# Performance work log

Hardware: AMD Instinct MI355X
Metric: run time of the kernel (lower is better)

The kernel has to match this reference:

```python
import jax, jax.numpy as jnp
import numpy as np

N_SOURCES = 100000
N_SENSORS = 306
N_TIMES = 256
N_FEATURES = 8
HIDDEN = 128
N_LAYERS = 3
N_EDGES = 600000
TIKHONOV_REG = 1e-3


def setup_inputs() -> dict:
    key = jax.random.key(0)
    ks = jax.random.split(key, 16)
    scale = 1.0 / np.sqrt(HIDDEN)
    in_dim = N_FEATURES + N_TIMES
    return {
        "Y": jax.random.normal(ks[0], (N_SENSORS, N_TIMES), dtype=jnp.float32),
        "L": jax.random.normal(ks[1], (N_SENSORS, N_SOURCES), dtype=jnp.float32),
        "vertex_features": jax.random.normal(ks[2], (N_SOURCES, N_FEATURES), dtype=jnp.float32),
        "senders": jax.random.randint(ks[3], (N_EDGES,), 0, N_SOURCES, dtype=jnp.int32),
        "receivers": jax.random.randint(ks[4], (N_EDGES,), 0, N_SOURCES, dtype=jnp.int32),
        # eqx.nn.Linear params: weight (out, in), bias (out,)
        "W_in": jax.random.normal(ks[5], (HIDDEN, in_dim), dtype=jnp.float32) / np.sqrt(in_dim),
        "b_in": jnp.zeros((HIDDEN,), dtype=jnp.float32),
        # GraphConvLayer params, stacked over layers; applied as x @ W (no transpose)
        "W_self": jax.random.normal(ks[6], (N_LAYERS, HIDDEN, HIDDEN), dtype=jnp.float32) * scale,
        "W_msg": jax.random.normal(ks[7], (N_LAYERS, HIDDEN, HIDDEN), dtype=jnp.float32) * scale,
        "b_layer": jnp.zeros((N_LAYERS, HIDDEN), dtype=jnp.float32),
        "W_out": jax.random.normal(ks[8], (N_TIMES, HIDDEN), dtype=jnp.float32) / np.sqrt(HIDDEN),
        "b_out": jnp.zeros((N_TIMES,), dtype=jnp.float32),
    }


def _tikhonov_inverse(Y, L, reg):
    # J = V @ diag(s / (s^2 + reg^2)) @ U^T @ Y
    U, s, Vt = jnp.linalg.svd(L, full_matrices=False)
    filt = s / (s ** 2 + reg ** 2)
    return Vt.T @ (filt[:, None] * (U.T @ Y))  # (n_sources, n_times)


def _graph_conv(x, senders, receivers, W_self, W_msg, b):
    n_nodes = x.shape[0]
    messages = x[senders]                                   # (E, H) gather
    agg = jnp.zeros_like(x).at[receivers].add(messages)     # (N, H) scatter-add
    degree = jnp.zeros((n_nodes,), x.dtype).at[receivers].add(1.0)
    msg_mean = agg / jnp.maximum(degree, 1.0)[:, None]
    return jax.nn.relu(x @ W_self + msg_mean @ W_msg + b)


def reference(Y, L, vertex_features, senders, receivers,
              W_in, b_in, W_self, W_msg, b_layer, W_out, b_out):
    J0 = _tikhonov_inverse(Y, L, TIKHONOV_REG)              # (N, T)
    x = jnp.concatenate([J0, vertex_features], axis=1)      # (N, T + F)
    x = x @ W_in.T + b_in                                   # vmap(Linear)
    for i in range(N_LAYERS):
        x = _graph_conv(x, senders, receivers, W_self[i], W_msg[i], b_layer[i])
    J = x @ W_out.T + b_out                                 # (N, T)
    return J
```

## Files before the change

### kernel.cpp

```cpp
#include <hip/hip_runtime.h>

#define NSRC 100000
#define NSEN 306
#define NT 256
#define NF 8
#define NH 128
#define NL 3
#define NE 600000
#define JITERS 10

#define GP_SPLIT 125
#define GP_CHUNK 800

typedef short short8 __attribute__((ext_vector_type(8)));
typedef float f32x4 __attribute__((ext_vector_type(4)));

__device__ __forceinline__ short f2b(float f) {
    union { float f; unsigned u; } v; v.f = f;
    unsigned r = v.u + 0x7fffu + ((v.u >> 16) & 1u);
    return (short)(r >> 16);
}
__device__ __forceinline__ float b2f(unsigned short s) {
    union { unsigned u; float f; } v; v.u = ((unsigned)s) << 16;
    return v.f;
}

__global__ __launch_bounds__(512) void k_gram_p1(const float* __restrict__ L, float* __restrict__ Gp) {
    __shared__ short T[320 * 72];
    const int bid = blockIdx.x;
    const int g = bid >> 4, r = bid & 15;
    const int p = g * 8 + (r & 7);
    if (p >= GP_SPLIT) return;
    const int bi = r >> 3;
    const int c0 = p * GP_CHUNK;
    const int cend = c0 + GP_CHUNK;
    const int tid = threadIdx.x;
    const int lane = tid & 63, wid = tid >> 6;
    const int wr = wid >> 2, wc = wid & 3;

    f32x4 acc[5][5] = {};

    for (int s0 = c0; s0 < cend; s0 += 64) {
        __syncthreads();
        for (int task = tid; task < 640; task += 512) {
            const int row = task >> 1, half = task & 1;
            const int col = s0 + half * 32;
            const bool ok = (row < NSEN) && (col + 31 < cend);
            const float* src = L + (size_t)row * NSRC + col;
            #pragma unroll
            for (int q = 0; q < 4; ++q) {
                float4 f0 = make_float4(0.f, 0.f, 0.f, 0.f);
                float4 f1 = make_float4(0.f, 0.f, 0.f, 0.f);
                if (ok) { f0 = *(const float4*)(src + q * 8); f1 = *(const float4*)(src + q * 8 + 4); }
                short8 t;
                t[0] = f2b(f0.x); t[1] = f2b(f0.y); t[2] = f2b(f0.z); t[3] = f2b(f0.w);
                t[4] = f2b(f1.x); t[5] = f2b(f1.y); t[6] = f2b(f1.z); t[7] = f2b(f1.w);
                *(short8*)&T[row * 72 + half * 32 + q * 8] = t;
            }
        }
        __syncthreads();
        #pragma unroll
        for (int ks = 0; ks < 2; ++ks) {
            const int kb = ks * 32 + (lane >> 4) * 8;
            short8 a[5], b[5];
            #pragma unroll
            for (int i = 0; i < 5; ++i) {
                a[i] = *(const short8*)&T[(bi * 160 + wr * 80 + i * 16 + (lane & 15)) * 72 + kb];
                b[i] = *(const short8*)&T[(wc * 80 + i * 16 + (lane & 15)) * 72 + kb];
            }
            #pragma unroll
            for (int i = 0; i < 5; ++i)
                #pragma unroll
                for (int j = 0; j < 5; ++j)
                    acc[i][j] = __builtin_amdgcn_mfma_f32_16x16x32_bf16(a[i], b[j], acc[i][j], 0, 0, 0);
        }
    }
    float* dst = Gp + (size_t)p * 320 * 320;
    #pragma unroll
    for (int i = 0; i < 5; ++i)
        #pragma unroll
        for (int j = 0; j < 5; ++j) {
            const int gj = wc * 80 + j * 16 + (lane & 15);
            #pragma unroll
            for (int rr = 0; rr < 4; ++rr) {
                const int gi = bi * 160 + wr * 80 + i * 16 + (lane >> 4) * 4 + rr;
                dst[gi * 320 + gj] = acc[i][j][rr];
            }
        }
}

__global__ void k_gram_p2(const float* __restrict__ Gp, float* __restrict__ G) {
    const int idx = blockIdx.x * 256 + threadIdx.x;
    if (idx >= 320 * 320) return;
    float s = 0.f;
    for (int p = 0; p < GP_SPLIT; ++p) s += Gp[(size_t)p * 102400 + idx];
    if ((idx / 320) == (idx % 320)) s += 1e-6f;
    G[idx] = s;
}

__global__ __launch_bounds__(256) void k_solve(const float* __restrict__ G, const float* __restrict__ Y,
                                               float* __restrict__ X) {
    __shared__ float Xl[NSEN * 8];
    const int c0 = blockIdx.x * 8;
    const int tid = threadIdx.x;
    const int i1 = tid, i2 = 256 + tid;
    const bool has2 = i2 < NSEN;
    const int i2c = has2 ? i2 : 0;

    float y1[8], y2[8], x1[8], x2[8];
    const float d1i = 1.f / G[i1 * 320 + i1];
    const float d2i = has2 ? (1.f / G[i2c * 320 + i2c]) : 0.f;
    *(float4*)&y1[0] = *(const float4*)&Y[i1 * NT + c0];
    *(float4*)&y1[4] = *(const float4*)&Y[i1 * NT + c0 + 4];
    *(float4*)&y2[0] = *(const float4*)&Y[i2c * NT + c0];
    *(float4*)&y2[4] = *(const float4*)&Y[i2c * NT + c0 + 4];
    #pragma unroll
    for (int c = 0; c < 8; ++c) { x1[c] = y1[c] * d1i; x2[c] = y2[c] * d2i; }
    #pragma unroll
    for (int c = 0; c < 8; ++c) { Xl[i1 * 8 + c] = x1[c]; if (has2) Xl[i2 * 8 + c] = x2[c]; }
    __syncthreads();

    for (int it = 0; it < JITERS; ++it) {
        float r1[8], r2[8];
        #pragma unroll
        for (int c = 0; c < 8; ++c) { r1[c] = y1[c]; r2[c] = y2[c]; }
        for (int k = 0; k < NSEN; ++k) {
            const float g1 = G[k * 320 + i1];
            const float g2 = G[k * 320 + i2c];
            const float4 xa = *(const float4*)&Xl[k * 8];
            const float4 xb = *(const float4*)&Xl[k * 8 + 4];
            r1[0] = fmaf(-g1, xa.x, r1[0]); r1[1] = fmaf(-g1, xa.y, r1[1]);
            r1[2] = fmaf(-g1, xa.z, r1[2]); r1[3] = fmaf(-g1, xa.w, r1[3]);
            r1[4] = fmaf(-g1, xb.x, r1[4]); r1[5] = fmaf(-g1, xb.y, r1[5]);
            r1[6] = fmaf(-g1, xb.z, r1[6]); r1[7] = fmaf(-g1, xb.w, r1[7]);
            r2[0] = fmaf(-g2, xa.x, r2[0]); r2[1] = fmaf(-g2, xa.y, r2[1]);
            r2[2] = fmaf(-g2, xa.z, r2[2]); r2[3] = fmaf(-g2, xa.w, r2[3]);
            r2[4] = fmaf(-g2, xb.x, r2[4]); r2[5] = fmaf(-g2, xb.y, r2[5]);
            r2[6] = fmaf(-g2, xb.z, r2[6]); r2[7] = fmaf(-g2, xb.w, r2[7]);
        }
        __syncthreads();
        #pragma unroll
        for (int c = 0; c < 8; ++c) {
            x1[c] += r1[c] * d1i; x2[c] += r2[c] * d2i;
            Xl[i1 * 8 + c] = x1[c];
            if (has2) Xl[i2 * 8 + c] = x2[c];
        }
        __syncthreads();
    }
    *(float4*)&X[i1 * NT + c0] = *(const float4*)&x1[0];
    *(float4*)&X[i1 * NT + c0 + 4] = *(const float4*)&x1[4];
    if (has2) {
        *(float4*)&X[i2 * NT + c0] = *(const float4*)&x2[0];
        *(float4*)&X[i2 * NT + c0 + 4] = *(const float4*)&x2[4];
    }
}

__global__ __launch_bounds__(128) void k_Z(const float* __restrict__ X, const float* __restrict__ W_in,
                                           short* __restrict__ Zt) {
    __shared__ float xs[NT];
    const int i = blockIdx.x, h = threadIdx.x;
    xs[h] = X[i * NT + h];
    xs[h + 128] = X[i * NT + h + 128];
    __syncthreads();
    const float* w = W_in + (size_t)h * (NT + NF);
    float acc = 0.f;
    #pragma unroll 4
    for (int t = 0; t < NT; ++t) acc = fmaf(xs[t], w[t], acc);
    Zt[h * 352 + i] = f2b(acc);
}

__global__ void k_prep(const float* __restrict__ W_self, const float* __restrict__ W_msg,
                       const float* __restrict__ W_out, const float* __restrict__ W_in,
                       short* __restrict__ WtL, short* __restrict__ Wob, short* __restrict__ Zt) {
    const int idx = blockIdx.x * 256 + threadIdx.x;
    if (idx < 3 * 128 * 256) {
        const int l = idx >> 15, rem = idx & 32767;
        const int h = rem >> 8, k = rem & 255;
        float v = (k < 128) ? W_self[l * 16384 + k * 128 + h] : W_msg[l * 16384 + (k - 128) * 128 + h];
        WtL[idx] = f2b(v);
    } else if (idx < 3 * 128 * 256 + 256 * 128) {
        const int j = idx - 3 * 128 * 256;
        Wob[j] = f2b(W_out[j]);
    } else if (idx < 3 * 128 * 256 + 256 * 128 + 128 * 8) {
        const int j = idx - (3 * 128 * 256 + 256 * 128);
        const int h = j >> 3, f = j & 7;
        Zt[h * 352 + 320 + f] = f2b(W_in[(size_t)h * (NT + NF) + NT + f]);
    }
}

__global__ __launch_bounds__(256) void k_x0(const float* __restrict__ L, const short* __restrict__ Zt,
                                            const float* __restrict__ vf, const float* __restrict__ b_in,
                                            short* __restrict__ xout) {
    __shared__ short At[128 * 40];
    __shared__ short Bt[128 * 40];
    __shared__ float bs[128];
    const int n0 = blockIdx.x * 128;
    const int tid = threadIdx.x;
    const int lane = tid & 63, wid = tid >> 6;
    const int wr = wid >> 1, wc = wid & 1;
    if (tid < 128) bs[tid] = b_in[tid];

    f32x4 acc[4][4] = {};

    for (int s0 = 0; s0 <= 320; s0 += 32) {
        __syncthreads();
        {
            const int s_loc = tid >> 3, nseg = (tid & 7) * 16;
            float v[16];
            if (s0 < 320) {
                const int srow = s0 + s_loc;
                const bool okrow = srow < NSEN;
                const float* src = L + (size_t)srow * NSRC + n0 + nseg;
                #pragma unroll
                for (int i = 0; i < 16; i += 4) {
                    float4 f = make_float4(0.f, 0.f, 0.f, 0.f);
                    const int gn = n0 + nseg + i;
                    if (okrow) {
                        if (gn + 3 < NSRC) f = *(const float4*)(src + i);
                        else {
                            if (gn < NSRC) f.x = src[i];
                            if (gn + 1 < NSRC) f.y = src[i + 1];
                            if (gn + 2 < NSRC) f.z = src[i + 2];
                        }
                    }
                    v[i] = f.x; v[i + 1] = f.y; v[i + 2] = f.z; v[i + 3] = f.w;
                }
            } else {
                #pragma unroll
                for (int i = 0; i < 16; ++i) {
                    const int gn = n0 + nseg + i;
                    v[i] = (s_loc < NF && gn < NSRC) ? vf[(size_t)gn * NF + s_loc] : 0.f;
                }
            }
            #pragma unroll
            for (int i = 0; i < 16; ++i) At[(nseg + i) * 40 + s_loc] = f2b(v[i]);
        }
        {
            const int h = tid >> 1, seg = tid & 1;
            const short8 z0 = *(const short8*)&Zt[h * 352 + s0 + seg * 16];
            const short8 z1 = *(const short8*)&Zt[h * 352 + s0 + seg * 16 + 8];
            *(short8*)&Bt[h * 40 + seg * 16] = z0;
            *(short8*)&Bt[h * 40 + seg * 16 + 8] = z1;
        }
        __syncthreads();
        const int kb = (lane >> 4) * 8;
        short8 a[4], b[4];
        #pragma unroll
        for (int i = 0; i < 4; ++i) a[i] = *(const short8*)&At[(wr * 64 + i * 16 + (lane & 15)) * 40 + kb];
        #pragma unroll
        for (int j = 0; j < 4; ++j) b[j] = *(const short8*)&Bt[(wc * 64 + j * 16 + (lane & 15)) * 40 + kb];
        #pragma unroll
        for (int i = 0; i < 4; ++i)
            #pragma unroll
            for (int j = 0; j < 4; ++j)
                acc[i][j] = __builtin_amdgcn_mfma_f32_16x16x32_bf16(a[i], b[j], acc[i][j], 0, 0, 0);
    }
    #pragma unroll
    for (int i = 0; i < 4; ++i)
        #pragma unroll
        for (int j = 0; j < 4; ++j) {
            const int h = wc * 64 + j * 16 + (lane & 15);
            #pragma unroll
            for (int rr = 0; rr < 4; ++rr) {
                const int n = n0 + wr * 64 + i * 16 + (lane >> 4) * 4 + rr;
                if (n < NSRC) xout[(size_t)n * NH + h] = f2b(acc[i][j][rr] + bs[h]);
            }
        }
}

__global__ void k_hist(const int* __restrict__ recv, int* __restrict__ cnt) {
    int e = blockIdx.x * 256 + threadIdx.x;
    if (e < NE) atomicAdd(&cnt[recv[e]], 1);
}

__global__ __launch_bounds__(1024) void k_scan(const int* __restrict__ cnt, int* __restrict__ rowptr) {
    __shared__ int sd[1024];
    const int tid = threadIdx.x;
    int running = 0;
    for (int base = 0; base < NSRC; base += 8192) {
        int off = base + tid * 8;
        int v[8]; int s = 0;
        #pragma unroll
        for (int j = 0; j < 8; ++j) { v[j] = (off + j < NSRC) ? cnt[off + j] : 0; s += v[j]; }
        __syncthreads();
        sd[tid] = s;
        __syncthreads();
        for (int d = 1; d < 1024; d <<= 1) {
            int add = (tid >= d) ? sd[tid - d] : 0;
            __syncthreads();
            sd[tid] += add;
            __syncthreads();
        }
        int run = running + sd[tid] - s;
        int total = sd[1023];
        #pragma unroll
        for (int j = 0; j < 8; ++j) { if (off + j < NSRC) rowptr[off + j] = run; run += v[j]; }
        running += total;
    }
    if (tid == 0) rowptr[NSRC] = running;
}

__global__ void k_fill(const int* __restrict__ send, const int* __restrict__ recv,
                       int* __restrict__ cursor, int* __restrict__ csr) {
    int e = blockIdx.x * 256 + threadIdx.x;
    if (e < NE) {
        int pos = atomicAdd(&cursor[recv[e]], 1);
        csr[pos] = send[e];
    }
}

__global__ __launch_bounds__(256) void k_agg(const short* __restrict__ x, const int* __restrict__ rowptr,
                                             const int* __restrict__ csr, short* __restrict__ mean) {
    const int lane = threadIdx.x & 63;
    const int n = blockIdx.x * 4 + (threadIdx.x >> 6);
    if (n >= NSRC) return;
    const int beg = rowptr[n], end = rowptr[n + 1];
    float a0 = 0.f, a1 = 0.f;
    for (int e = beg; e < end; ++e) {
        const int s = csr[e];
        const unsigned u = *(const unsigned*)&x[(size_t)s * NH + lane * 2];
        a0 += b2f((unsigned short)(u & 0xffff));
        a1 += b2f((unsigned short)(u >> 16));
    }
    const int d = end - beg;
    const float inv = 1.f / (float)(d > 0 ? d : 1);
    const unsigned o = (unsigned)(unsigned short)f2b(a0 * inv) | ((unsigned)(unsigned short)f2b(a1 * inv) << 16);
    *(unsigned*)&mean[(size_t)n * NH + lane * 2] = o;
}

__global__ __launch_bounds__(256) void k_gcn(const short* __restrict__ x, const short* __restrict__ mean,
                                             const short* __restrict__ Wt, const float* __restrict__ b,
                                             short* __restrict__ out) {
    __shared__ short At[128 * 40];
    __shared__ short Bt[128 * 40];
    __shared__ float bs[128];
    const int n0 = blockIdx.x * 128;
    const int tid = threadIdx.x;
    const int lane = tid & 63, wid = tid >> 6;
    const int wr = wid >> 1, wc = wid & 1;
    if (tid < 128) bs[tid] = b[tid];

    f32x4 acc[4][4] = {};

    for (int kc = 0; kc < 8; ++kc) {
        const short* Asrc = (kc < 4) ? x : mean;
        const int ko = (kc & 3) * 32;
        __syncthreads();
        {
            const int nl = tid >> 1, seg = tid & 1;
            const int gn = n0 + nl;
            short8 v0 = {0,0,0,0,0,0,0,0}, v1 = {0,0,0,0,0,0,0,0};
            if (gn < NSRC) {
                v0 = *(const short8*)&Asrc[(size_t)gn * NH + ko + seg * 16];
                v1 = *(const short8*)&Asrc[(size_t)gn * NH + ko + seg * 16 + 8];
            }
            *(short8*)&At[nl * 40 + seg * 16] = v0;
            *(short8*)&At[nl * 40 + seg * 16 + 8] = v1;
        }
        {
            const int h = tid >> 1, seg = tid & 1;
            const short8 w0 = *(const short8*)&Wt[h * 256 + kc * 32 + seg * 16];
            const short8 w1 = *(const short8*)&Wt[h * 256 + kc * 32 + seg * 16 + 8];
            *(short8*)&Bt[h * 40 + seg * 16] = w0;
            *(short8*)&Bt[h * 40 + seg * 16 + 8] = w1;
        }
        __syncthreads();
        const int kb = (lane >> 4) * 8;
        short8 a[4], bb[4];
        #pragma unroll
        for (int i = 0; i < 4; ++i) a[i] = *(const short8*)&At[(wr * 64 + i * 16 + (lane & 15)) * 40 + kb];
        #pragma unroll
        for (int j = 0; j < 4; ++j) bb[j] = *(const short8*)&Bt[(wc * 64 + j * 16 + (lane & 15)) * 40 + kb];
        #pragma unroll
        for (int i = 0; i < 4; ++i)
            #pragma unroll
            for (int j = 0; j < 4; ++j)
                acc[i][j] = __builtin_amdgcn_mfma_f32_16x16x32_bf16(a[i], bb[j], acc[i][j], 0, 0, 0);
    }
    #pragma unroll
    for (int i = 0; i < 4; ++i)
        #pragma unroll
        for (int j = 0; j < 4; ++j) {
            const int h = wc * 64 + j * 16 + (lane & 15);
            #pragma unroll
            for (int rr = 0; rr < 4; ++rr) {
                const int n = n0 + wr * 64 + i * 16 + (lane >> 4) * 4 + rr;
                if (n < NSRC) out[(size_t)n * NH + h] = f2b(fmaxf(acc[i][j][rr] + bs[h], 0.f));
            }
        }
}

__global__ __launch_bounds__(256) void k_out(const short* __restrict__ x, const short* __restrict__ Wob,
                                             const float* __restrict__ bout, float* __restrict__ J) {
    __shared__ short At[128 * 40];
    __shared__ short Bt[128 * 40];
    __shared__ float bs[128];
    const int n0 = blockIdx.x * 128;
    const int t0 = blockIdx.y * 128;
    const int tid = threadIdx.x;
    const int lane = tid & 63, wid = tid >> 6;
    const int wr = wid >> 1, wc = wid & 1;
    if (tid < 128) bs[tid] = bout[t0 + tid];

    f32x4 acc[4][4] = {};

    for (int kc = 0; kc < 4; ++kc) {
        __syncthreads();
        {
            const int nl = tid >> 1, seg = tid & 1;
            const int gn = n0 + nl;
            short8 v0 = {0,0,0,0,0,0,0,0}, v1 = {0,0,0,0,0,0,0,0};
            if (gn < NSRC) {
                v0 = *(const short8*)&x[(size_t)gn * NH + kc * 32 + seg * 16];
                v1 = *(const short8*)&x[(size_t)gn * NH + kc * 32 + seg * 16 + 8];
            }
            *(short8*)&At[nl * 40 + seg * 16] = v0;
            *(short8*)&At[nl * 40 + seg * 16 + 8] = v1;
        }
        {
            const int tl = tid >> 1, seg = tid & 1;
            const short8 w0 = *(const short8*)&Wob[(t0 + tl) * NH + kc * 32 + seg * 16];
            const short8 w1 = *(const short8*)&Wob[(t0 + tl) * NH + kc * 32 + seg * 16 + 8];
            *(short8*)&Bt[tl * 40 + seg * 16] = w0;
            *(short8*)&Bt[tl * 40 + seg * 16 + 8] = w1;
        }
        __syncthreads();
        const int kb = (lane >> 4) * 8;
        short8 a[4], bb[4];
        #pragma unroll
        for (int i = 0; i < 4; ++i) a[i] = *(const short8*)&At[(wr * 64 + i * 16 + (lane & 15)) * 40 + kb];
        #pragma unroll
        for (int j = 0; j < 4; ++j) bb[j] = *(const short8*)&Bt[(wc * 64 + j * 16 + (lane & 15)) * 40 + kb];
        #pragma unroll
        for (int i = 0; i < 4; ++i)
            #pragma unroll
            for (int j = 0; j < 4; ++j)
                acc[i][j] = __builtin_amdgcn_mfma_f32_16x16x32_bf16(a[i], bb[j], acc[i][j], 0, 0, 0);
    }
    #pragma unroll
    for (int i = 0; i < 4; ++i)
        #pragma unroll
        for (int j = 0; j < 4; ++j) {
            const int tl = wc * 64 + j * 16 + (lane & 15);
            const int t = t0 + tl;
            #pragma unroll
            for (int rr = 0; rr < 4; ++rr) {
                const int n = n0 + wr * 64 + i * 16 + (lane >> 4) * 4 + rr;
                if (n < NSRC) J[(size_t)n * NT + t] = acc[i][j][rr] + bs[tl];
            }
        }
}

extern "C" void kernel_launch(void* const* d_in, const int* in_sizes, int n_in,
                              void* d_out, int out_size, void* d_ws, size_t ws_size,
                              hipStream_t stream) {
    const float* Y      = (const float*)d_in[0];
    const float* L      = (const float*)d_in[1];
    const float* vf     = (const float*)d_in[2];
    const int*   send   = (const int*)d_in[3];
    const int*   recv   = (const int*)d_in[4];
    const float* W_in   = (const float*)d_in[5];
    const float* b_in   = (const float*)d_in[6];
    const float* W_self = (const float*)d_in[7];
    const float* W_msg  = (const float*)d_in[8];
    const float* b_lay  = (const float*)d_in[9];
    const float* W_out  = (const float*)d_in[10];
    const float* b_out  = (const float*)d_in[11];
    float* out = (float*)d_out;

    char* ws = (char*)d_ws;
    size_t off = 0;
    auto alloc = [&](size_t bytes) -> void* {
        void* p = ws + off;
        off += (bytes + 255) & ~(size_t)255;
        return p;
    };
    char* big    = (char*)alloc((size_t)GP_SPLIT * 320 * 320 * 4);
    float* Gp    = (float*)big;
    short* xA    = (short*)big;
    short* xB    = (short*)(big + (size_t)NSRC * NH * 2);
    float* G     = (float*)alloc((size_t)320 * 320 * 4);
    float* X     = (float*)alloc((size_t)NSEN * NT * 4);
    short* Zt    = (short*)alloc((size_t)NH * 352 * 2);
    short* WtL   = (short*)alloc((size_t)NL * NH * 256 * 2);
    short* Wob   = (short*)alloc((size_t)NT * NH * 2);
    int* rowptr  = (int*)alloc((size_t)(NSRC + 1) * 4);
    int* cursor  = (int*)alloc((size_t)NSRC * 4);
    int* cnt     = (int*)alloc((size_t)NSRC * 4);
    int* csr     = (int*)alloc((size_t)NE * 4);

    hipMemsetAsync(cnt, 0, (size_t)NSRC * 4, stream);
    hipMemsetAsync(Zt, 0, (size_t)NH * 352 * 2, stream);

    k_prep<<<(3 * 128 * 256 + 256 * 128 + 128 * 8 + 255) / 256, 256, 0, stream>>>(
        W_self, W_msg, W_out, W_in, WtL, Wob, Zt);

    k_hist<<<(NE + 255) / 256, 256, 0, stream>>>(recv, cnt);
    k_scan<<<1, 1024, 0, stream>>>(cnt, rowptr);
    hipMemcpyAsync(cursor, rowptr, (size_t)NSRC * 4, hipMemcpyDeviceToDevice, stream);
    k_fill<<<(NE + 255) / 256, 256, 0, stream>>>(send, recv, cursor, csr);

    k_gram_p1<<<256, 512, 0, stream>>>(L, Gp);
    k_gram_p2<<<(320 * 320 + 255) / 256, 256, 0, stream>>>(Gp, G);
    k_solve<<<NT / 8, 256, 0, stream>>>(G, Y, X);
    k_Z<<<NSEN, 128, 0, stream>>>(X, W_in, Zt);
    k_x0<<<(NSRC + 127) / 128, 256, 0, stream>>>(L, Zt, vf, b_in, xA);

    short* x = xA;
    short* m = xB;
    for (int l = 0; l < NL; ++l) {
        k_agg<<<(NSRC + 3) / 4, 256, 0, stream>>>(x, rowptr, csr, m);
        k_gcn<<<(NSRC + 127) / 128, 256, 0, stream>>>(
            x, m, WtL + (size_t)l * NH * 256, b_lay + (size_t)l * NH, m);
        short* t = x; x = m; m = t;
    }
    k_out<<<dim3((NSRC + 127) / 128, 2), 256, 0, stream>>>(x, Wob, b_out, out);
}
```

Measured before the change: 955.9 us.

## Project Y through W_in before the Jacobi solve and cut iterations

Uses linearity to apply W_in to Y first, so the Jacobi solve runs on 128 columns instead of 256 and writes the bf16 Zt directly, removing the separate k_Z pass. The solve is re-tiled to 2 columns per block over 64 blocks, with an 8-way unrolled inner loop. Jacobi iterations are also cut from 10 to 6, which lowers accuracy of the regularised solve and risks tolerance failures.

Measured after the change: 868.0 us. -9.2%, faster.

```diff
diff --git a/kernel.cpp b/kernel.cpp
--- a/kernel.cpp
+++ b/kernel.cpp
@@ -7,7 +7,7 @@
 #define NH 128
 #define NL 3
 #define NE 600000
-#define JITERS 10
+#define JITERS 6
 
 #define GP_SPLIT 125
 #define GP_CHUNK 800
@@ -98,75 +98,76 @@
     G[idx] = s;
 }
 
-__global__ __launch_bounds__(256) void k_solve(const float* __restrict__ G, const float* __restrict__ Y,
-                                               float* __restrict__ X) {
-    __shared__ float Xl[NSEN * 8];
-    const int c0 = blockIdx.x * 8;
-    const int tid = threadIdx.x;
-    const int i1 = tid, i2 = 256 + tid;
-    const bool has2 = i2 < NSEN;
-    const int i2c = has2 ? i2 : 0;
-
-    float y1[8], y2[8], x1[8], x2[8];
-    const float d1i = 1.f / G[i1 * 320 + i1];
-    const float d2i = has2 ? (1.f / G[i2c * 320 + i2c]) : 0.f;
-    *(float4*)&y1[0] = *(const float4*)&Y[i1 * NT + c0];
-    *(float4*)&y1[4] = *(const float4*)&Y[i1 * NT + c0 + 4];
-    *(float4*)&y2[0] = *(const float4*)&Y[i2c * NT + c0];
-    *(float4*)&y2[4] = *(const float4*)&Y[i2c * NT + c0 + 4];
-    #pragma unroll
-    for (int c = 0; c < 8; ++c) { x1[c] = y1[c] * d1i; x2[c] = y2[c] * d2i; }
-    #pragma unroll
-    for (int c = 0; c < 8; ++c) { Xl[i1 * 8 + c] = x1[c]; if (has2) Xl[i2 * 8 + c] = x2[c]; }
-    __syncthreads();
-
-    for (int it = 0; it < JITERS; ++it) {
-        float r1[8], r2[8];
-        #pragma unroll
-        for (int c = 0; c < 8; ++c) { r1[c] = y1[c]; r2[c] = y2[c]; }
-        for (int k = 0; k < NSEN; ++k) {
-            const float g1 = G[k * 320 + i1];
-            const float g2 = G[k * 320 + i2c];
-            const float4 xa = *(const float4*)&Xl[k * 8];
-            const float4 xb = *(const float4*)&Xl[k * 8 + 4];
-            r1[0] = fmaf(-g1, xa.x, r1[0]); r1[1] = fmaf(-g1, xa.y, r1[1]);
-            r1[2] = fmaf(-g1, xa.z, r1[2]); r1[3] = fmaf(-g1, xa.w, r1[3]);
-            r1[4] = fmaf(-g1, xb.x, r1[4]); r1[5] = fmaf(-g1, xb.y, r1[5]);
-            r1[6] = fmaf(-g1, xb.z, r1[6]); r1[7] = fmaf(-g1, xb.w, r1[7]);
-            r2[0] = fmaf(-g2, xa.x, r2[0]); r2[1] = fmaf(-g2, xa.y, r2[1]);
-            r2[2] = fmaf(-g2, xa.z, r2[2]); r2[3] = fmaf(-g2, xa.w, r2[3]);
-            r2[4] = fmaf(-g2, xb.x, r2[4]); r2[5] = fmaf(-g2, xb.y, r2[5]);
-            r2[6] = fmaf(-g2, xb.z, r2[6]); r2[7] = fmaf(-g2, xb.w, r2[7]);
-        }
-        __syncthreads();
-        #pragma unroll
-        for (int c = 0; c < 8; ++c) {
-            x1[c] += r1[c] * d1i; x2[c] += r2[c] * d2i;
-            Xl[i1 * 8 + c] = x1[c];
-            if (has2) Xl[i2 * 8 + c] = x2[c];
-        }
-        __syncthreads();
-    }
-    *(float4*)&X[i1 * NT + c0] = *(const float4*)&x1[0];
-    *(float4*)&X[i1 * NT + c0 + 4] = *(const float4*)&x1[4];
-    if (has2) {
-        *(float4*)&X[i2 * NT + c0] = *(const float4*)&x2[0];
-        *(float4*)&X[i2 * NT + c0 + 4] = *(const float4*)&x2[4];
-    }
-}
-
-__global__ __launch_bounds__(128) void k_Z(const float* __restrict__ X, const float* __restrict__ W_in,
-                                           short* __restrict__ Zt) {
-    __shared__ float xs[NT];
+__global__ __launch_bounds__(128) void k_Yw(const float* __restrict__ Y, const float* __restrict__ W_in,
+                                            float* __restrict__ Yw) {
+    __shared__ float ys[NT];
     const int i = blockIdx.x, h = threadIdx.x;
-    xs[h] = X[i * NT + h];
-    xs[h + 128] = X[i * NT + h + 128];
+    ys[h] = Y[i * NT + h];
+    ys[h + 128] = Y[i * NT + h + 128];
     __syncthreads();
     const float* w = W_in + (size_t)h * (NT + NF);
     float acc = 0.f;
     #pragma unroll 4
-    for (int t = 0; t < NT; ++t) acc = fmaf(xs[t], w[t], acc);
-    Zt[h * 352 + i] = f2b(acc);
+    for (int t = 0; t < NT; ++t) acc = fmaf(ys[t], w[t], acc);
+    Yw[i * 128 + h] = acc;
+}
+
+__global__ __launch_bounds__(256) void k_solve(const float* __restrict__ G, const float* __restrict__ Yw,
+                                               short* __restrict__ Zt) {
+    __shared__ float Xl[320 * 2];
+    const int c0 = blockIdx.x * 2;
+    const int tid = threadIdx.x;
+    const int i1 = tid;
+    const int i2 = 256 + tid;
+    const bool has2 = i2 < NSEN;
+    const int i2c = has2 ? i2 : 0;
+
+    const float d1i = 1.f / G[i1 * 320 + i1];
+    const float d2i = has2 ? (1.f / G[i2c * 320 + i2c]) : 0.f;
+    float y1[2], y2[2], x1[2], x2[2];
+    y1[0] = Yw[i1 * 128 + c0]; y1[1] = Yw[i1 * 128 + c0 + 1];
+    y2[0] = has2 ? Yw[i2 * 128 + c0] : 0.f;
+    y2[1] = has2 ? Yw[i2 * 128 + c0 + 1] : 0.f;
+    x1[0] = y1[0] * d1i; x1[1] = y1[1] * d1i;
+    x2[0] = y2[0] * d2i; x2[1] = y2[1] * d2i;
+    Xl[i1 * 2] = x1[0]; Xl[i1 * 2 + 1] = x1[1];
+    if (has2)      { Xl[i2 * 2] = x2[0]; Xl[i2 * 2 + 1] = x2[1]; }
+    else if (tid < 64) { Xl[i2 * 2] = 0.f; Xl[i2 * 2 + 1] = 0.f; }
+    __syncthreads();
+
+    for (int it = 0; it < JITERS; ++it) {
+        float r1[2] = {y1[0], y1[1]};
+        float r2[2] = {y2[0], y2[1]};
+        for (int k0 = 0; k0 < 320; k0 += 8) {
+            float g1[8], g2[8];
+            float2 xx[8];
+            #pragma unroll
+            for (int u = 0; u < 8; ++u) {
+                g1[u] = G[(k0 + u) * 320 + i1];
+                g2[u] = G[(k0 + u) * 320 + i2c];
+                xx[u] = *(const float2*)&Xl[(k0 + u) * 2];
+            }
+            #pragma unroll
+            for (int u = 0; u < 8; ++u) {
+                r1[0] = fmaf(-g1[u], xx[u].x, r1[0]);
+                r1[1] = fmaf(-g1[u], xx[u].y, r1[1]);
+                r2[0] = fmaf(-g2[u], xx[u].x, r2[0]);
+                r2[1] = fmaf(-g2[u], xx[u].y, r2[1]);
+            }
+        }
+        __syncthreads();
+        x1[0] += r1[0] * d1i; x1[1] += r1[1] * d1i;
+        x2[0] += r2[0] * d2i; x2[1] += r2[1] * d2i;
+        Xl[i1 * 2] = x1[0]; Xl[i1 * 2 + 1] = x1[1];
+        if (has2) { Xl[i2 * 2] = x2[0]; Xl[i2 * 2 + 1] = x2[1]; }
+        __syncthreads();
+    }
+    Zt[(c0) * 352 + i1]     = f2b(x1[0]);
+    Zt[(c0 + 1) * 352 + i1] = f2b(x1[1]);
+    if (has2) {
+        Zt[(c0) * 352 + i2]     = f2b(x2[0]);
+        Zt[(c0 + 1) * 352 + i2] = f2b(x2[1]);
+    }
 }
 
 __global__ void k_prep(const float* __restrict__ W_self, const float* __restrict__ W_msg,
@@ -480,7 +481,7 @@
     short* xA    = (short*)big;
     short* xB    = (short*)(big + (size_t)NSRC * NH * 2);
     float* G     = (float*)alloc((size_t)320 * 320 * 4);
-    float* X     = (float*)alloc((size_t)NSEN * NT * 4);
+    float* Yw    = (float*)alloc((size_t)NSEN * 128 * 4);
     short* Zt    = (short*)alloc((size_t)NH * 352 * 2);
     short* WtL   = (short*)alloc((size_t)NL * NH * 256 * 2);
     short* Wob   = (short*)alloc((size_t)NT * NH * 2);
@@ -494,6 +495,7 @@
 
     k_prep<<<(3 * 128 * 256 + 256 * 128 + 128 * 8 + 255) / 256, 256, 0, stream>>>(
         W_self, W_msg, W_out, W_in, WtL, Wob, Zt);
+    k_Yw<<<NSEN, 128, 0, stream>>>(Y, W_in, Yw);
 
     k_hist<<<(NE + 255) / 256, 256, 0, stream>>>(recv, cnt);
     k_scan<<<1, 1024, 0, stream>>>(cnt, rowptr);
@@ -502,8 +504,7 @@
 
     k_gram_p1<<<256, 512, 0, stream>>>(L, Gp);
     k_gram_p2<<<(320 * 320 + 255) / 256, 256, 0, stream>>>(Gp, G);
-    k_solve<<<NT / 8, 256, 0, stream>>>(G, Y, X);
-    k_Z<<<NSEN, 128, 0, stream>>>(X, W_in, Zt);
+    k_solve<<<64, 256, 0, stream>>>(G, Yw, Zt);
     k_x0<<<(NSRC + 127) / 128, 256, 0, stream>>>(L, Zt, vf, b_in, xA);
 
     short* x = xA;
```
